# Optimization experiments

Hardware: AMD Instinct MI355X
Metric: run time of the kernel (lower is better)

Reference implementation:

```python
import jax, jax.numpy as jnp
import numpy as np


def setup_inputs() -> dict:
    key = jax.random.key(0)
    k1, k2 = jax.random.split(key)
    inp = jax.random.uniform(k1, (4096, 512), dtype=jnp.float32)  # non-negative features
    # FlyHash sparse binary projection: each of the 10240 output rows connects
    # to nb_proj_entries=6 random input features.
    proj_idx = jax.random.randint(k2, (10240, 6), 0, 512)
    return {"inp": inp, "proj_idx": proj_idx, "hash_length": 32}


def reference(inp, proj_idx, hash_length):
    # Build the sparse binary projection as a dense [out_features, in_features]
    # matrix (20 MB) and use a single GEMM -- same math as torch.sparse.mm.
    out_features = proj_idx.shape[0]
    rows = jnp.arange(out_features)[:, None]  # [out, 1]
    W = jnp.zeros((out_features, inp.shape[1]), dtype=inp.dtype).at[rows, proj_idx].add(1.0)
    act = inp @ W.T  # [batch, out_features]
    # MB_sparsify: per-row winner-take-all, keep the hash_length largest
    # activations, zero the rest (returned dense instead of scipy COO).
    kth = jax.lax.top_k(act, hash_length)[0][:, -1:]  # kth-largest per row
    return jnp.where(act >= kth, act, jnp.zeros((), dtype=act.dtype))
```

## Files before the change

### kernel.cpp

```cpp
#include <hip/hip_runtime.h>

#define IN_F     512
#define OUT_F    10240
#define NPROJ    6
#define THREADS  512
#define PER_T    (OUT_F / THREADS)
#define ROWS     4
#define NBINS    256
#define CAND_CAP 128
#define NWAVES   (THREADS / 64)
#define BIN_OFF  8064u

typedef float    float4v __attribute__((ext_vector_type(4)));
typedef unsigned uint4v  __attribute__((ext_vector_type(4)));

__global__ __launch_bounds__(THREADS, 4) void flyhash_wta_kernel(
    const float* __restrict__ inp,
    const int*   __restrict__ proj,
    const int*   __restrict__ hlen,
    float*       __restrict__ out,
    int batch)
{
    __shared__ float4v  s_rowT[IN_F];
    __shared__ unsigned s_hist[ROWS][NBINS];
    __shared__ unsigned s_bin[ROWS];
    __shared__ float    s_cand[ROWS][CAND_CAP];
    __shared__ unsigned s_cnt[ROWS];
    __shared__ float    s_kth[ROWS];
    __shared__ int      s_pc[ROWS][NWAVES];

    const int t    = threadIdx.x;
    const int lane = t & 63;
    const int wave = t >> 6;
    const int b0   = blockIdx.x * ROWS;

    {
        const int r  = t & 3;
        const int cb = t >> 2;
        int br = b0 + r;
        if (br >= batch) br = batch - 1;
        const float* g = inp + (size_t)br * IN_F;
#pragma unroll
        for (int p = 0; p < 4; ++p) {
            const int c = cb + p * (THREADS / 4);
            ((float*)s_rowT)[c * 4 + r] = g[c];
        }
    }
    ((unsigned*)s_hist)[t]           = 0u;
    ((unsigned*)s_hist)[t + THREADS] = 0u;
    if (t < ROWS) { s_cnt[t] = 0u; s_kth[t] = 0.0f; }
    __syncthreads();

    const int k0 = hlen[0];

    float4v acc[PER_T];
#pragma unroll
    for (int i = 0; i < PER_T; ++i) {
        const int o = t + i * THREADS;
        const int2* ip = (const int2*)(proj + (size_t)o * NPROJ);
        const int2 p0 = ip[0];
        const int2 p1 = ip[1];
        const int2 p2 = ip[2];
        const float4v a01 = s_rowT[p0.x] + s_rowT[p0.y];
        const float4v a23 = s_rowT[p1.x] + s_rowT[p1.y];
        const float4v a45 = s_rowT[p2.x] + s_rowT[p2.y];
        acc[i] = (a01 + a23) + a45;
    }

    float4v tmax = acc[0];
#pragma unroll
    for (int i = 1; i < PER_T; ++i) {
        tmax.x = fmaxf(tmax.x, acc[i].x);
        tmax.y = fmaxf(tmax.y, acc[i].y);
        tmax.z = fmaxf(tmax.z, acc[i].z);
        tmax.w = fmaxf(tmax.w, acc[i].w);
    }

#pragma unroll
    for (int r = 0; r < ROWS; ++r) {
        int key = (int)(__float_as_uint(tmax[r]) >> 17) - (int)BIN_OFF;
        key = key < 0 ? 0 : (key > NBINS - 1 ? NBINS - 1 : key);
        atomicAdd(&s_hist[r][key], 1u);
    }
    __syncthreads();

    if (wave < ROWS) {
        const uint4v h = ((const uint4v*)&s_hist[wave][0])[lane];
        const unsigned s3 = h.w;
        const unsigned s2 = h.z + s3;
        const unsigned s1 = h.y + s2;
        const unsigned s0 = h.x + s1;
        unsigned T = s0;
#pragma unroll
        for (int d = 1; d < 64; d <<= 1) {
            const unsigned o = __shfl_down(T, d);
            if (lane + d < 64) T += o;
        }
        const unsigned A = T - s0;
        const unsigned S0 = A + s0, S1 = A + s1, S2 = A + s2, S3 = A + s3;
        if (h.x && (int)S0 >= k0 && (int)(S0 - h.x) < k0) s_bin[wave] = 4u * lane + 0u;
        if (h.y && (int)S1 >= k0 && (int)(S1 - h.y) < k0) s_bin[wave] = 4u * lane + 1u;
        if (h.z && (int)S2 >= k0 && (int)(S2 - h.z) < k0) s_bin[wave] = 4u * lane + 2u;
        if (h.w && (int)S3 >= k0 && (int)(S3 - h.w) < k0) s_bin[wave] = 4u * lane + 3u;
        if (lane == 0 && (int)(A + s0) < k0) s_bin[wave] = 0u;
    }
    __syncthreads();

    float4v T4;
#pragma unroll
    for (int r = 0; r < ROWS; ++r) {
        const unsigned B = s_bin[r];
        T4[r] = (B == 0u) ? 0.0f : __uint_as_float((B + BIN_OFF) << 17);
    }

#pragma unroll
    for (int i = 0; i < PER_T; ++i) {
#pragma unroll
        for (int r = 0; r < ROWS; ++r) {
            const float v = acc[i][r];
            if (v >= T4[r]) {
                const unsigned idx = atomicAdd(&s_cnt[r], 1u);
                if (idx < CAND_CAP) s_cand[r][idx] = v;
            }
        }
    }
    __syncthreads();

    unsigned ovf = 0;
#pragma unroll
    for (int r = 0; r < ROWS; ++r)
        if (s_cnt[r] > CAND_CAP) ovf |= (1u << r);

    if (ovf) {
        unsigned lo[ROWS], hi[ROWS];
#pragma unroll
        for (int r = 0; r < ROWS; ++r) {
            lo[r] = __float_as_uint(T4[r]);
            hi[r] = 0x41000000u;
        }
        for (int it = 0; it < 34; ++it) {
            unsigned work = 0;
#pragma unroll
            for (int r = 0; r < ROWS; ++r)
                if (((ovf >> r) & 1u) && hi[r] - lo[r] > 1u) work |= (1u << r);
            if (!work) break;
            unsigned mid[ROWS];
#pragma unroll
            for (int r = 0; r < ROWS; ++r) mid[r] = lo[r] + (hi[r] - lo[r]) / 2u;
            int c0 = 0, c1 = 0, c2 = 0, c3 = 0;
#pragma unroll
            for (int i = 0; i < PER_T; ++i) {
                c0 += (__float_as_uint(acc[i].x) >= mid[0]);
                c1 += (__float_as_uint(acc[i].y) >= mid[1]);
                c2 += (__float_as_uint(acc[i].z) >= mid[2]);
                c3 += (__float_as_uint(acc[i].w) >= mid[3]);
            }
#pragma unroll
            for (int d = 1; d < 64; d <<= 1) {
                c0 += __shfl_xor(c0, d);
                c1 += __shfl_xor(c1, d);
                c2 += __shfl_xor(c2, d);
                c3 += __shfl_xor(c3, d);
            }
            if (lane == 0) {
                s_pc[0][wave] = c0; s_pc[1][wave] = c1;
                s_pc[2][wave] = c2; s_pc[3][wave] = c3;
            }
            __syncthreads();
#pragma unroll
            for (int r = 0; r < ROWS; ++r) {
                if ((work >> r) & 1u) {
                    int c = 0;
#pragma unroll
                    for (int w = 0; w < NWAVES; ++w) c += s_pc[r][w];
                    if (c >= k0) lo[r] = mid[r]; else hi[r] = mid[r];
                }
            }
            __syncthreads();
        }
        if (t == 0) {
#pragma unroll
            for (int r = 0; r < ROWS; ++r)
                if ((ovf >> r) & 1u) s_kth[r] = __uint_as_float(lo[r]);
        }
    }

    if (wave < ROWS && !((ovf >> wave) & 1u)) {
        const unsigned c = s_cnt[wave];
        for (unsigned s = lane; s < c; s += 64) {
            const float v = s_cand[wave][s];
            int gt = 0, eq = 0;
            for (unsigned j = 0; j < c; ++j) {
                const float u = s_cand[wave][j];
                gt += (u > v);
                eq += (u == v);
            }
            if (gt < k0 && gt + eq >= k0) s_kth[wave] = v;
        }
    }
    __syncthreads();
    const float4v kth4 = { s_kth[0], s_kth[1], s_kth[2], s_kth[3] };

#pragma unroll
    for (int r = 0; r < ROWS; ++r) {
        const int br = b0 + r;
        if (br < batch) {
            float* orow = out + (size_t)br * OUT_F;
#pragma unroll
            for (int i = 0; i < PER_T; ++i) {
                const float v = acc[i][r];
                orow[t + i * THREADS] = (v >= kth4[r]) ? v : 0.0f;
            }
        }
    }
}

extern "C" void kernel_launch(void* const* d_in, const int* in_sizes, int n_in,
                              void* d_out, int out_size, void* d_ws, size_t ws_size,
                              hipStream_t stream) {
    const float* inp  = (const float*)d_in[0];
    const int*   proj = (const int*)d_in[1];
    const int*   hlen = (const int*)d_in[2];
    float*       out  = (float*)d_out;

    const int batch  = in_sizes[0] / IN_F;
    const int blocks = (batch + ROWS - 1) / ROWS;

    hipLaunchKernelGGL(flyhash_wta_kernel, dim3(blocks), dim3(THREADS), 0, stream,
                       inp, proj, hlen, out, batch);
}
```

Baseline: 52.89 us.

## Compute histogram threshold per-wave via ballot, write zeros early, avoid barrier drains

Every wave now does the histogram prefix-scan for all four rows itself and locates the threshold bin with ballots, which removes the shared s_bin handoff and one block barrier. Outputs below the histogram threshold are written as zeros right away in the candidate pass, so their global stores overlap the kth-value selection. The final pass only stores the candidates above the threshold. Remaining __syncthreads are swapped for a barrier that waits only on LDS (lgkmcnt), so pending global stores are not drained at each barrier. The cost is redundant scan work in every wave and more scattered, divergent stores.

```diff
diff --git a/kernel.cpp b/kernel.cpp
--- a/kernel.cpp
+++ b/kernel.cpp
@@ -14,6 +14,12 @@
 typedef float    float4v __attribute__((ext_vector_type(4)));
 typedef unsigned uint4v  __attribute__((ext_vector_type(4)));
 
+__device__ __forceinline__ void bar_nodrain() {
+    asm volatile("s_waitcnt lgkmcnt(0)" ::: "memory");
+    __builtin_amdgcn_s_barrier();
+    __builtin_amdgcn_sched_barrier(0);
+}
+
 __global__ __launch_bounds__(THREADS, 4) void flyhash_wta_kernel(
     const float* __restrict__ inp,
     const int*   __restrict__ proj,
@@ -23,7 +29,6 @@
 {
     __shared__ float4v  s_rowT[IN_F];
     __shared__ unsigned s_hist[ROWS][NBINS];
-    __shared__ unsigned s_bin[ROWS];
     __shared__ float    s_cand[ROWS][CAND_CAP];
     __shared__ unsigned s_cnt[ROWS];
     __shared__ float    s_kth[ROWS];
@@ -84,8 +89,10 @@
     }
     __syncthreads();
 
-    if (wave < ROWS) {
-        const uint4v h = ((const uint4v*)&s_hist[wave][0])[lane];
+    float4v T4;
+#pragma unroll
+    for (int r = 0; r < ROWS; ++r) {
+        const uint4v h = ((const uint4v*)&s_hist[r][0])[lane];
         const unsigned s3 = h.w;
         const unsigned s2 = h.z + s3;
         const unsigned s1 = h.y + s2;
@@ -98,18 +105,21 @@
         }
         const unsigned A = T - s0;
         const unsigned S0 = A + s0, S1 = A + s1, S2 = A + s2, S3 = A + s3;
-        if (h.x && (int)S0 >= k0 && (int)(S0 - h.x) < k0) s_bin[wave] = 4u * lane + 0u;
-        if (h.y && (int)S1 >= k0 && (int)(S1 - h.y) < k0) s_bin[wave] = 4u * lane + 1u;
-        if (h.z && (int)S2 >= k0 && (int)(S2 - h.z) < k0) s_bin[wave] = 4u * lane + 2u;
-        if (h.w && (int)S3 >= k0 && (int)(S3 - h.w) < k0) s_bin[wave] = 4u * lane + 3u;
-        if (lane == 0 && (int)(A + s0) < k0) s_bin[wave] = 0u;
-    }
-    __syncthreads();
-
-    float4v T4;
-#pragma unroll
-    for (int r = 0; r < ROWS; ++r) {
-        const unsigned B = s_bin[r];
+        const bool cx = h.x && (int)S0 >= k0 && (int)(S0 - h.x) < k0;
+        const bool cy = h.y && (int)S1 >= k0 && (int)(S1 - h.y) < k0;
+        const bool cz = h.z && (int)S2 >= k0 && (int)(S2 - h.z) < k0;
+        const bool cw = h.w && (int)S3 >= k0 && (int)(S3 - h.w) < k0;
+        const unsigned long long bx = __ballot(cx);
+        const unsigned long long by = __ballot(cy);
+        const unsigned long long bz = __ballot(cz);
+        const unsigned long long bw = __ballot(cw);
+        const unsigned long long ball = bx | by | bz | bw;
+        unsigned B = 0u;
+        if (ball) {
+            const int L = __ffsll((long long)ball) - 1;
+            const unsigned long long m = 1ull << L;
+            B = 4u * (unsigned)L + ((bx & m) ? 0u : (by & m) ? 1u : (bz & m) ? 2u : 3u);
+        }
         T4[r] = (B == 0u) ? 0.0f : __uint_as_float((B + BIN_OFF) << 17);
     }
 
@@ -118,13 +128,17 @@
 #pragma unroll
         for (int r = 0; r < ROWS; ++r) {
             const float v = acc[i][r];
-            if (v >= T4[r]) {
+            if (v < T4[r]) {
+                const int br = b0 + r;
+                if (br < batch)
+                    out[(size_t)br * OUT_F + t + i * THREADS] = 0.0f;
+            } else {
                 const unsigned idx = atomicAdd(&s_cnt[r], 1u);
                 if (idx < CAND_CAP) s_cand[r][idx] = v;
             }
         }
     }
-    __syncthreads();
+    bar_nodrain();
 
     unsigned ovf = 0;
 #pragma unroll
@@ -166,7 +180,7 @@
                 s_pc[0][wave] = c0; s_pc[1][wave] = c1;
                 s_pc[2][wave] = c2; s_pc[3][wave] = c3;
             }
-            __syncthreads();
+            bar_nodrain();
 #pragma unroll
             for (int r = 0; r < ROWS; ++r) {
                 if ((work >> r) & 1u) {
@@ -176,7 +190,7 @@
                     if (c >= k0) lo[r] = mid[r]; else hi[r] = mid[r];
                 }
             }
-            __syncthreads();
+            bar_nodrain();
         }
         if (t == 0) {
 #pragma unroll
@@ -198,18 +212,19 @@
             if (gt < k0 && gt + eq >= k0) s_kth[wave] = v;
         }
     }
-    __syncthreads();
+    bar_nodrain();
     const float4v kth4 = { s_kth[0], s_kth[1], s_kth[2], s_kth[3] };
 
 #pragma unroll
-    for (int r = 0; r < ROWS; ++r) {
-        const int br = b0 + r;
-        if (br < batch) {
-            float* orow = out + (size_t)br * OUT_F;
-#pragma unroll
-            for (int i = 0; i < PER_T; ++i) {
-                const float v = acc[i][r];
-                orow[t + i * THREADS] = (v >= kth4[r]) ? v : 0.0f;
+    for (int i = 0; i < PER_T; ++i) {
+#pragma unroll
+        for (int r = 0; r < ROWS; ++r) {
+            const float v = acc[i][r];
+            if (v >= T4[r]) {
+                const int br = b0 + r;
+                if (br < batch)
+                    out[(size_t)br * OUT_F + t + i * THREADS]
+                        = (v >= kth4[r]) ? v : 0.0f;
             }
         }
     }
```

After: 103.3 us. 95.2% more time.
